# Kernel optimization log

Hardware: AMD Instinct MI355X
Metric: run time of the kernel (lower is better)

## Reference

```python
import jax, jax.numpy as jnp
import numpy as np
import math

D = 2048
H = 16
DH = D // H
DFF = 8192
B = 4
S = 2048
EPS = 1e-12


def gelu(x):
    # faithful tanh-approx gelu from source
    return 0.5 * x * (1.0 + jnp.tanh(math.sqrt(2.0 / math.pi) * (x + 0.044715 * x ** 3)))


def global_layernorm(x, w, b):
    # torch.mean(x)/torch.var(x): scalar mean and UNBIASED variance over ALL elements
    mean = jnp.mean(x)
    var = jnp.var(x, ddof=1)
    return (x - mean) / jnp.sqrt(var + EPS) * w + b


def setup_inputs() -> dict:
    key = jax.random.key(0)
    ks = jax.random.split(key, 12)
    sd = 0.02
    return {
        "x": jax.random.normal(ks[0], (B, S, D), jnp.float32),
        "W1_w": jax.random.normal(ks[1], (3 * D, D), jnp.float32) * sd,
        "W1_b": jnp.zeros((3 * D,), jnp.float32),
        "W2_w": jax.random.normal(ks[2], (D, D), jnp.float32) * sd,
        "W2_b": jnp.zeros((D,), jnp.float32),
        "fc_w": jax.random.normal(ks[3], (DFF, D), jnp.float32) * sd,
        "fc_b": jnp.zeros((DFF,), jnp.float32),
        "proj_w": jax.random.normal(ks[4], (D, DFF), jnp.float32) * sd,
        "proj_b": jnp.zeros((D,), jnp.float32),
        "ln1_w": jnp.ones((D,), jnp.float32),
        "ln1_b": jnp.zeros((D,), jnp.float32),
        "ln2_w": jnp.ones((D,), jnp.float32),
        "ln2_b": jnp.zeros((D,), jnp.float32),
    }


def attn(x, W1_w, W1_b, W2_w, W2_b):
    X = x @ W1_w.T + W1_b                     # [B,S,3D]
    Q, K, V = jnp.split(X, 3, axis=2)         # each [B,S,D]
    # reshape(): view (B,S,H,Dh) then permute
    q = Q.reshape(B, S, H, DH).transpose(0, 2, 3, 1)  # [B,H,Dh,S]
    k = K.reshape(B, S, H, DH).transpose(0, 2, 1, 3)  # [B,H,S,Dh]
    v = V.reshape(B, S, H, DH).transpose(0, 2, 3, 1)  # [B,H,Dh,S]
    # heads(): scores over head-feature dim, scaled by sqrt(q.size(-1)) = sqrt(S)
    w = jnp.einsum('bhds,bhse->bhde', q, k) / math.sqrt(S)  # [B,H,Dh,Dh]
    w = jax.nn.softmax(w, axis=-1)
    out = jnp.einsum('bhde,bhes->bhds', w, v)  # [B,H,Dh,S]
    # cat(): raw contiguous view [B,H,Dh,S] -> [B,S,H*Dh] (memory-order reshape)
    out = out.reshape(B, S, H * DH)
    return out @ W2_w.T + W2_b


def ffn(x, fc_w, fc_b, proj_w, proj_b):
    h = gelu(x @ fc_w.T + fc_b)
    return h @ proj_w.T + proj_b


def reference(x, W1_w, W1_b, W2_w, W2_b, fc_w, fc_b, proj_w, proj_b,
              ln1_w, ln1_b, ln2_w, ln2_b):
    a = attn(x, W1_w, W1_b, W2_w, W2_b)
    x = global_layernorm(a + x, ln1_w, ln1_b)
    m = ffn(x, fc_w, fc_b, proj_w, proj_b)
    x = global_layernorm(m + x, ln2_w, ln2_b)
    return x
```

## Files before the change

kernel.cpp:

```cpp
#include <hip/hip_runtime.h>
#include <math.h>

typedef float floatx4 __attribute__((ext_vector_type(4)));
typedef __bf16 bf16x8 __attribute__((ext_vector_type(8)));
typedef unsigned short ushortx8 __attribute__((ext_vector_type(8)));
typedef unsigned short ushortx4 __attribute__((ext_vector_type(4)));
typedef unsigned short ushortx2 __attribute__((ext_vector_type(2)));

typedef unsigned int __attribute__((address_space(1))) as1_uint;
typedef unsigned int __attribute__((address_space(3))) as3_uint;

#define DEV static __device__ __forceinline__

DEV unsigned short f32_bf16(float f) {
  unsigned u = __float_as_uint(f);
  u += 0x7FFFu + ((u >> 16) & 1u);
  return (unsigned short)(u >> 16);
}
DEV float bf16_f32(unsigned short h) { return __uint_as_float(((unsigned)h) << 16); }
DEV float gelu_f(float x) {
  float x3 = x * x * x;
  return 0.5f * x * (1.0f + tanhf(0.79788456080286536f * (x + 0.044715f * x3)));
}
DEV void gload16(const void* g, void* l) {
  __builtin_amdgcn_global_load_lds((const as1_uint*)g, (as3_uint*)l, 16, 0, 0);
}
DEV floatx4 mfma16(ushortx8 a, ushortx8 b, floatx4 c) {
  return __builtin_amdgcn_mfma_f32_16x16x32_bf16(
      __builtin_bit_cast(bf16x8, a), __builtin_bit_cast(bf16x8, b), c, 0, 0, 0);
}


__global__ void zero_f(float* p, int n) {
  int i = threadIdx.x;
  if (i < n) p[i] = 0.f;
}

__global__ void cvt_f32_bf16(const float* __restrict__ in, unsigned short* __restrict__ out,
                             long n4) {
  long i = (long)blockIdx.x * blockDim.x + threadIdx.x;
  if (i >= n4) return;
  float4 v = ((const float4*)in)[i];
  ushortx4 o;
  o.x = f32_bf16(v.x); o.y = f32_bf16(v.y); o.z = f32_bf16(v.z); o.w = f32_bf16(v.w);
  ((ushortx4*)out)[i] = o;
}

__global__ void cvt_cols(const float* __restrict__ in, unsigned short* __restrict__ out,
                         int cbase, int cwlog4, long n4) {
  long i = (long)blockIdx.x * blockDim.x + threadIdx.x;
  if (i >= n4) return;
  int n = (int)(i >> cwlog4);
  int k4 = (int)(i & ((1 << cwlog4) - 1)) << 2;
  float4 v = *(const float4*)&in[(size_t)n * 8192 + cbase + k4];
  ushortx4 o;
  o.x = f32_bf16(v.x); o.y = f32_bf16(v.y); o.z = f32_bf16(v.z); o.w = f32_bf16(v.w);
  *(ushortx4*)&out[((size_t)n << (cwlog4 + 2)) + k4] = o;
}

__global__ __launch_bounds__(256) void softmax_k(const float* __restrict__ sc,
                                                 unsigned short* __restrict__ probs) {
  int r = blockIdx.x * 4 + (threadIdx.x >> 6);
  int lane = threadIdx.x & 63;
  size_t base = (size_t)(r >> 7) * 16384 + (size_t)(r & 127) * 128;
  int e0 = lane * 2;
  float2 p = *(const float2*)&sc[base + e0];
  const float scale = 0.022097086912079608f;
  float vx = p.x * scale, vy = p.y * scale;
  float m = fmaxf(vx, vy);
#pragma unroll
  for (int off = 32; off; off >>= 1) m = fmaxf(m, __shfl_xor(m, off));
  float ex = expf(vx - m), ey = expf(vy - m);
  float s = ex + ey;
#pragma unroll
  for (int off = 32; off; off >>= 1) s += __shfl_xor(s, off);
  float inv = 1.f / s;
  ushortx2 o;
  o.x = f32_bf16(ex * inv);
  o.y = f32_bf16(ey * inv);
  *(ushortx2*)&probs[base + e0] = o;
}

__global__ void ln_apply(const float* __restrict__ r, const float* __restrict__ stats,
                         const float* __restrict__ w, const float* __restrict__ bia,
                         float* __restrict__ outF, unsigned short* __restrict__ outB, long n4) {
  long i = (long)blockIdx.x * blockDim.x + threadIdx.x;
  if (i >= n4) return;
  const double total = 16777216.0;
  double mean = (double)stats[0] / total;
  double var = ((double)stats[1] - total * mean * mean) / (total - 1.0);
  float rstd = (float)(1.0 / sqrt(var + 1e-12));
  float fm = (float)mean;
  int col = (int)((i * 4) & 2047);
  float4 v = ((const float4*)r)[i];
  float4 wv = *(const float4*)&w[col];
  float4 bv = *(const float4*)&bia[col];
  float4 o;
  o.x = (v.x - fm) * rstd * wv.x + bv.x;
  o.y = (v.y - fm) * rstd * wv.y + bv.y;
  o.z = (v.z - fm) * rstd * wv.z + bv.z;
  o.w = (v.w - fm) * rstd * wv.w + bv.w;
  if (outF) ((float4*)outF)[i] = o;
  if (outB) {
    ushortx4 ob;
    ob.x = f32_bf16(o.x); ob.y = f32_bf16(o.y); ob.z = f32_bf16(o.z); ob.w = f32_bf16(o.w);
    ((ushortx4*)outB)[i] = ob;
  }
}

__global__ __launch_bounds__(256) void gemm_bt(
    const unsigned short* __restrict__ A, int lda, long sAo, long sAi,
    const unsigned short* __restrict__ B, int ldb, long sBo, long sBi,
    int K, int innerCnt,
    const float* __restrict__ bias, const float* __restrict__ residF,
    const unsigned short* __restrict__ residB, int accum,
    float* __restrict__ outF, unsigned short* __restrict__ outB,
    unsigned short* __restrict__ outQT,
    int ldc, long sCo, long sCi, int doGelu, float* __restrict__ stats) {
  __shared__ unsigned short As[128 * 64];
  __shared__ unsigned short Bs[128 * 64];
  const int tid = threadIdx.x;
  const int wave = tid >> 6;
  const int lane = tid & 63;
  const int z = blockIdx.z;
  const int zo = z / innerCnt, zi = z % innerCnt;
  const unsigned short* Ab = A + zo * sAo + zi * sAi;
  const unsigned short* Bb = B + zo * sBo + zi * sBi;
  const long coff = zo * sCo + zi * sCi;
  const int m0 = blockIdx.y * 128;
  const int n0 = blockIdx.x * 128;

  const int quad = lane >> 4;
  const int l16 = lane & 15;
  const int wm = (wave & 1) * 64;
  const int wn = (wave >> 1) * 64;
  const int srow = lane >> 3;
  const int kofs8 = (((lane & 7) ^ srow) & 7) * 8;

  floatx4 acc[4][4];
#pragma unroll
  for (int i = 0; i < 4; i++)
#pragma unroll
    for (int j = 0; j < 4; j++) acc[i][j] = (floatx4){0.f, 0.f, 0.f, 0.f};

  const int nK = K >> 6;
  for (int kt = 0; kt < nK; ++kt) {
    const int k0 = kt << 6;
    __syncthreads();
#pragma unroll
    for (int i = 0; i < 4; ++i) {
      const int rb = wave * 32 + i * 8;
      gload16(Ab + (size_t)(m0 + rb + srow) * lda + k0 + kofs8, &As[rb * 64]);
      gload16(Bb + (size_t)(n0 + rb + srow) * ldb + k0 + kofs8, &Bs[rb * 64]);
    }
    __syncthreads();
#pragma unroll
    for (int kk = 0; kk < 2; ++kk) {
      ushortx8 af[4], bf[4];
      const int swz = (l16 & 7);
#pragma unroll
      for (int i = 0; i < 4; i++)
        af[i] = *(const ushortx8*)&As[(wm + i * 16 + l16) * 64 +
                                      (((kk * 4 + quad) ^ swz) * 8)];
#pragma unroll
      for (int j = 0; j < 4; j++)
        bf[j] = *(const ushortx8*)&Bs[(wn + j * 16 + l16) * 64 +
                                      (((kk * 4 + quad) ^ swz) * 8)];
#pragma unroll
      for (int i = 0; i < 4; i++)
#pragma unroll
        for (int j = 0; j < 4; j++) acc[i][j] = mfma16(af[i], bf[j], acc[i][j]);
    }
  }

  float s1 = 0.f, s2 = 0.f;
#pragma unroll
  for (int i = 0; i < 4; i++) {
#pragma unroll
    for (int j = 0; j < 4; j++) {
      const int col = n0 + wn + j * 16 + l16;
      const float bv = bias ? bias[col] : 0.f;
#pragma unroll
      for (int r = 0; r < 4; r++) {
        const int row = m0 + wm + i * 16 + quad * 4 + r;
        float v = acc[i][j][r] + bv;
        if (doGelu) v = gelu_f(v);
        if (outQT) {
          const int b = row >> 11, s = row & 2047;
          if (col < 4096) {
            unsigned short* tb = outQT + ((col & 2048) ? 16777216u : 0u);
            const int cc = col & 2047;
            tb[((size_t)((b << 4) + (cc >> 7)) * 128 + (cc & 127)) * 2048 + s] = f32_bf16(v);
          } else {
            outB[(size_t)row * 2048 + (col - 4096)] = f32_bf16(v);
          }
          continue;
        }
        const size_t cidx = (size_t)coff + (size_t)row * ldc + col;
        if (residF) v += residF[cidx];
        if (residB) v += bf16_f32(residB[cidx]);
        if (accum) v += outF[cidx];
        if (outF) outF[cidx] = v;
        else outB[cidx] = f32_bf16(v);
        if (stats) { s1 += v; s2 += v * v; }
      }
    }
  }
  if (stats) {
#pragma unroll
    for (int off = 32; off; off >>= 1) {
      s1 += __shfl_down(s1, off);
      s2 += __shfl_down(s2, off);
    }
    if (lane == 0) {
      atomicAdd(&stats[0], s1);
      atomicAdd(&stats[1], s2);
    }
  }
}

__global__ __launch_bounds__(512, 2) void gemm256(
    const unsigned short* __restrict__ A, int lda,
    const unsigned short* __restrict__ B, int ldb, int K,
    const float* __restrict__ bias, const float* __restrict__ residF,
    const unsigned short* __restrict__ residB, int accum,
    float* __restrict__ outF, unsigned short* __restrict__ outB,
    unsigned short* __restrict__ outQT, int ldc, int doGelu,
    float* __restrict__ stats) {
  __shared__ unsigned short As[2][256 * 64];
  __shared__ unsigned short Bs[2][256 * 64];
  const int tid = threadIdx.x;
  const int wave = tid >> 6;
  const int lane = tid & 63;
  const int wm = wave >> 2;
  const int wn = wave & 3;
  const int quad = lane >> 4;
  const int l16 = lane & 15;
  const int swz = l16 & 7;

  const int nwg = gridDim.x * gridDim.y;
  const int orig = blockIdx.y * gridDim.x + blockIdx.x;
  const int q8 = nwg >> 3, r8 = nwg & 7;
  const int xcd = orig & 7, lid = orig >> 3;
  const int wgid = (xcd < r8 ? xcd * (q8 + 1) : r8 * (q8 + 1) + (xcd - r8) * q8) + lid;
  const int m0 = (wgid / gridDim.x) * 256;
  const int n0 = (wgid % gridDim.x) * 256;

  const int srow = lane >> 3;
  const int kof = (((lane & 7) ^ srow) & 7) << 3;
  const int nkt = K >> 6;

  floatx4 acc[8][4];
#pragma unroll
  for (int i = 0; i < 8; i++)
#pragma unroll
    for (int j = 0; j < 4; j++) acc[i][j] = (floatx4){0.f, 0.f, 0.f, 0.f};

  auto slot = [&](int kt, int s) {
    const int buf = kt & 1;
    const int k0 = kt << 6;
    if (s < 2) {
      const int rb = s * 128 + wave * 16;
      gload16(B + (size_t)(n0 + rb + srow) * ldb + k0 + kof, &Bs[buf][rb * 64]);
      gload16(B + (size_t)(n0 + rb + 8 + srow) * ldb + k0 + kof, &Bs[buf][(rb + 8) * 64]);
    } else {
      const int rb = ((wave & 4) << 5) + ((wave & 3) << 4) + (s == 3 ? 64 : 0);
      gload16(A + (size_t)(m0 + rb + srow) * lda + k0 + kof, &As[buf][rb * 64]);
      gload16(A + (size_t)(m0 + rb + 8 + srow) * lda + k0 + kof, &As[buf][(rb + 8) * 64]);
    }
  };

  slot(0, 0); slot(0, 1); slot(0, 2); slot(0, 3);
  if (nkt > 1) { slot(1, 0); slot(1, 1); slot(1, 2); }
  asm volatile("s_waitcnt vmcnt(6)" ::: "memory");
  __builtin_amdgcn_s_barrier();
  asm volatile("" ::: "memory");

  ushortx8 bfr[4][2], afr[2][2];
  const int aBase = (wm * 128 + l16) * 64;
  const int bBase = (wn * 64 + l16) * 64;
  const int kq0 = (quad ^ swz) << 3;
  const int kq1 = ((4 + quad) ^ swz) << 3;

  for (int kt = 0; kt < nkt; kt += 2) {
#pragma unroll
    for (int half = 0; half < 2; half++) {
      const unsigned short* Asb = &As[half][0];
      const unsigned short* Bsb = &Bs[half][0];
#pragma unroll
      for (int p = 0; p < 4; p++) {
        if (p == 0) {
#pragma unroll
          for (int fj = 0; fj < 4; fj++) {
            bfr[fj][0] = *(const ushortx8*)&Bsb[bBase + fj * 1024 + kq0];
            bfr[fj][1] = *(const ushortx8*)&Bsb[bBase + fj * 1024 + kq1];
          }
        }
#pragma unroll
        for (int fi = 0; fi < 2; fi++) {
          afr[fi][0] = *(const ushortx8*)&Asb[aBase + (p * 2 + fi) * 1024 + kq0];
          afr[fi][1] = *(const ushortx8*)&Asb[aBase + (p * 2 + fi) * 1024 + kq1];
        }
        if (half == 0) {
          if (p == 0) { if (kt + 1 < nkt) slot(kt + 1, 3); }
          else { if (kt + 2 < nkt) slot(kt + 2, p - 1); }
        } else {
          if (p == 0) { if (kt + 2 < nkt) slot(kt + 2, 3); }
          else { if (kt + 3 < nkt) slot(kt + 3, p - 1); }
        }
        __builtin_amdgcn_s_barrier();
        asm volatile("s_waitcnt lgkmcnt(0)" ::: "memory");
        __builtin_amdgcn_s_setprio(1);
#pragma unroll
        for (int fi = 0; fi < 2; fi++)
#pragma unroll
          for (int fj = 0; fj < 4; fj++) {
            acc[p * 2 + fi][fj] = mfma16(afr[fi][0], bfr[fj][0], acc[p * 2 + fi][fj]);
            acc[p * 2 + fi][fj] = mfma16(afr[fi][1], bfr[fj][1], acc[p * 2 + fi][fj]);
          }
        __builtin_amdgcn_s_setprio(0);
        if (p == 3) {
          const bool more = (half == 0) ? (kt + 2 < nkt) : (kt + 3 < nkt);
          if (more) asm volatile("s_waitcnt vmcnt(6)" ::: "memory");
          else asm volatile("s_waitcnt vmcnt(0)" ::: "memory");
        }
        __builtin_amdgcn_s_barrier();
        asm volatile("" ::: "memory");
      }
    }
  }

  float s1 = 0.f, s2 = 0.f;
#pragma unroll
  for (int i = 0; i < 8; i++) {
#pragma unroll
    for (int j = 0; j < 4; j++) {
      const int col = n0 + wn * 64 + j * 16 + l16;
      const float bv = bias ? bias[col] : 0.f;
#pragma unroll
      for (int r = 0; r < 4; r++) {
        const int row = m0 + wm * 128 + i * 16 + quad * 4 + r;
        float v = acc[i][j][r] + bv;
        if (doGelu) v = gelu_f(v);
        if (outQT) {
          const int b = row >> 11, s = row & 2047;
          if (col < 4096) {
            unsigned short* tb = outQT + ((col & 2048) ? 16777216u : 0u);
            const int cc = col & 2047;
            tb[((size_t)((b << 4) + (cc >> 7)) * 128 + (cc & 127)) * 2048 + s] = f32_bf16(v);
          } else {
            outB[(size_t)row * 2048 + (col - 4096)] = f32_bf16(v);
          }
          continue;
        }
        const size_t cidx = (size_t)row * ldc + col;
        if (residF) v += residF[cidx];
        if (residB) v += bf16_f32(residB[cidx]);
        if (accum) v += outF[cidx];
        if (outF) outF[cidx] = v;
        else outB[cidx] = f32_bf16(v);
        if (stats) { s1 += v; s2 += v * v; }
      }
    }
  }
  if (stats) {
#pragma unroll
    for (int off = 32; off; off >>= 1) {
      s1 += __shfl_down(s1, off);
      s2 += __shfl_down(s2, off);
    }
    if (lane == 0) {
      atomicAdd(&stats[0], s1);
      atomicAdd(&stats[1], s2);
    }
  }
}


extern "C" void kernel_launch(void* const* d_in, const int* in_sizes, int n_in, void* d_out,
                              int out_size, void* d_ws, size_t ws_size, hipStream_t stream) {
  (void)in_sizes; (void)n_in; (void)out_size;
  const float* x    = (const float*)d_in[0];
  const float* W1w  = (const float*)d_in[1];
  const float* W1b  = (const float*)d_in[2];
  const float* W2w  = (const float*)d_in[3];
  const float* W2b  = (const float*)d_in[4];
  const float* fcw  = (const float*)d_in[5];
  const float* fcb  = (const float*)d_in[6];
  const float* pjw  = (const float*)d_in[7];
  const float* pjb  = (const float*)d_in[8];
  const float* ln1w = (const float*)d_in[9];
  const float* ln1b = (const float*)d_in[10];
  const float* ln2w = (const float*)d_in[11];
  const float* ln2b = (const float*)d_in[12];
  float* out = (float*)d_out;

  char* ws = (char*)d_ws;
  size_t off = 0;
  auto take = [&](size_t b) { size_t r = off; off = (off + b + 255) & ~(size_t)255; return r; };
  float* stats = (float*)(ws + take(256));
  size_t P0 = take(33554432);
  size_t P1 = take(25165824);
  size_t P2 = take(100663296);
  size_t P3 = off;

  unsigned short* xbf    = (unsigned short*)(ws + P0);
  unsigned short* attnbf = (unsigned short*)(ws + P0);
  unsigned short* W1bf   = (unsigned short*)(ws + P1);
  float*          spart  = (float*)(ws + P1);
  unsigned short* probs  = (unsigned short*)(ws + P1 + 4194304);
  unsigned short* W2bf   = (unsigned short*)(ws + P1);
  unsigned short* vbf    = (unsigned short*)(ws + P2);
  unsigned short* qT     = (unsigned short*)(ws + P2 + 33554432);
  float*          r12    = (float*)(ws + P2);
  unsigned short* x1bf   = (unsigned short*)(ws + P2 + 67108864);

  int nc;
  unsigned short *fc_ch, *pj_ch, *hch;
  if (ws_size >= P3 + 201326592) {
    nc = 1;
    fc_ch = (unsigned short*)(ws + P3);
    pj_ch = (unsigned short*)(ws + P3 + 33554432);
    hch   = (unsigned short*)(ws + P3 + 67108864);
  } else if (ws_size >= P3 + 100663296) {
    nc = 2;
    fc_ch = (unsigned short*)(ws + P3);
    pj_ch = (unsigned short*)(ws + P3 + 16777216);
    hch   = (unsigned short*)(ws + P3 + 33554432);
  } else {
    nc = 4;
    fc_ch = (unsigned short*)(ws + P1);
    pj_ch = (unsigned short*)(ws + P1 + 8388608);
    hch   = (unsigned short*)(ws + P0);
  }
  const int cw = 8192 / nc;
  const int cwlog4 = (nc == 1) ? 11 : (nc == 2) ? 10 : 9;
  const long cn4 = (long)cw << 9;

  zero_f<<<1, 64, 0, stream>>>(stats, 16);
  cvt_f32_bf16<<<16384, 256, 0, stream>>>(x, xbf, 4194304);
  cvt_f32_bf16<<<12288, 256, 0, stream>>>(W1w, W1bf, 3145728);

  gemm256<<<dim3(24, 32, 1), 512, 0, stream>>>(xbf, 2048, W1bf, 2048, 2048, W1b, nullptr,
                                               nullptr, 0, nullptr, vbf, qT, 0, 0, nullptr);
  gemm_bt<<<dim3(1, 1, 64), 256, 0, stream>>>(qT, 2048, 0, 262144L, qT + 16777216, 2048, 0,
                                              262144L, 2048, 64, nullptr, nullptr, nullptr, 0,
                                              spart, nullptr, nullptr, 128, 0, 16384L, 0, nullptr);
  softmax_k<<<2048, 256, 0, stream>>>(spart, probs);
  gemm_bt<<<dim3(16, 1, 64), 256, 0, stream>>>(probs, 128, 262144L, 16384L, vbf, 2048, 4194304L,
                                               128L, 128, 16, nullptr, nullptr, nullptr, 0,
                                               nullptr, attnbf, nullptr, 2048, 4194304L, 262144L,
                                               0, nullptr);
  cvt_f32_bf16<<<4096, 256, 0, stream>>>(W2w, W2bf, 1048576);
  gemm256<<<dim3(8, 32, 1), 512, 0, stream>>>(attnbf, 2048, W2bf, 2048, 2048, W2b, x, nullptr,
                                              0, r12, nullptr, nullptr, 2048, 0, stats);
  ln_apply<<<16384, 256, 0, stream>>>(r12, stats, ln1w, ln1b, nullptr, x1bf, 4194304);

  for (int c = 0; c < nc; ++c) {
    cvt_f32_bf16<<<(int)(cn4 / 256), 256, 0, stream>>>(fcw + (size_t)c * cw * 2048, fc_ch, cn4);
    cvt_cols<<<(int)(cn4 / 256), 256, 0, stream>>>(pjw, pj_ch, c * cw, cwlog4, cn4);
    gemm256<<<dim3(cw / 256, 32, 1), 512, 0, stream>>>(x1bf, 2048, fc_ch, 2048, 2048,
                                                       fcb + c * cw, nullptr, nullptr, 0,
                                                       nullptr, hch, nullptr, cw, 1, nullptr);
    const int last = (c == nc - 1);
    gemm256<<<dim3(8, 32, 1), 512, 0, stream>>>(hch, cw, pj_ch, cw, cw,
                                                last ? pjb : nullptr, nullptr,
                                                last ? x1bf : nullptr, c > 0, r12, nullptr,
                                                nullptr, 2048, 0,
                                                last ? (stats + 2) : nullptr);
  }
  ln_apply<<<16384, 256, 0, stream>>>(r12, stats + 2, ln2w, ln2b, out, nullptr, 4194304);
}
```

Measured before the change: 1.596 ms.

## Split-K score GEMM, LDS-transposed QKV epilogue, grouped tile order, finer vmcnt waits

Several independent changes. The Q·K^T score GEMM is split four ways along the sequence dimension (256 workgroups instead of 64), and the softmax kernel sums the four partial results. The QKV GEMM epilogue now transposes Q/K tiles through LDS so the transposed bf16 output is written as coalesced 16-byte stores instead of scattered 2-byte stores. The GEMM also gets a grouped tile-to-workgroup mapping for L2 reuse, finer-grained vmcnt waits with the lgkmcnt wait removed, and a sigmoid-form GELU using a fast exp and reciprocal. The risks are extra partial-score traffic and slightly different GELU rounding.

```diff
diff --git a/kernel.cpp b/kernel.cpp
--- a/kernel.cpp
+++ b/kernel.cpp
@@ -19,8 +19,8 @@
 }
 DEV float bf16_f32(unsigned short h) { return __uint_as_float(((unsigned)h) << 16); }
 DEV float gelu_f(float x) {
-  float x3 = x * x * x;
-  return 0.5f * x * (1.0f + tanhf(0.79788456080286536f * (x + 0.044715f * x3)));
+  float t2 = 1.5957691216057308f * (x + 0.044715f * x * x * x);
+  return x * __builtin_amdgcn_rcpf(1.0f + __expf(-t2));
 }
 DEV void gload16(const void* g, void* l) {
   __builtin_amdgcn_global_load_lds((const as1_uint*)g, (as3_uint*)l, 16, 0, 0);
@@ -62,11 +62,14 @@
                                                  unsigned short* __restrict__ probs) {
   int r = blockIdx.x * 4 + (threadIdx.x >> 6);
   int lane = threadIdx.x & 63;
-  size_t base = (size_t)(r >> 7) * 16384 + (size_t)(r & 127) * 128;
-  int e0 = lane * 2;
-  float2 p = *(const float2*)&sc[base + e0];
+  size_t base = (size_t)(r >> 7) * 16384 + (size_t)(r & 127) * 128 + lane * 2;
+  float2 p0 = *(const float2*)&sc[base];
+  float2 p1 = *(const float2*)&sc[base + 1048576];
+  float2 p2 = *(const float2*)&sc[base + 2097152];
+  float2 p3 = *(const float2*)&sc[base + 3145728];
   const float scale = 0.022097086912079608f;
-  float vx = p.x * scale, vy = p.y * scale;
+  float vx = (p0.x + p1.x + p2.x + p3.x) * scale;
+  float vy = (p0.y + p1.y + p2.y + p3.y) * scale;
   float m = fmaxf(vx, vy);
 #pragma unroll
   for (int off = 32; off; off >>= 1) m = fmaxf(m, __shfl_xor(m, off));
@@ -78,7 +81,7 @@
   ushortx2 o;
   o.x = f32_bf16(ex * inv);
   o.y = f32_bf16(ey * inv);
-  *(ushortx2*)&probs[base + e0] = o;
+  *(ushortx2*)&probs[base] = o;
 }
 
 __global__ void ln_apply(const float* __restrict__ r, const float* __restrict__ stats,
@@ -243,8 +246,15 @@
   const int q8 = nwg >> 3, r8 = nwg & 7;
   const int xcd = orig & 7, lid = orig >> 3;
   const int wgid = (xcd < r8 ? xcd * (q8 + 1) : r8 * (q8 + 1) + (xcd - r8) * q8) + lid;
-  const int m0 = (wgid / gridDim.x) * 256;
-  const int n0 = (wgid % gridDim.x) * 256;
+  int m0, n0;
+  if ((gridDim.x & 7) == 0) {
+    const int gper = (int)(gridDim.y << 3);
+    m0 = ((wgid % gper) >> 3) * 256;
+    n0 = (((wgid / gper) << 3) + (wgid & 7)) * 256;
+  } else {
+    m0 = (wgid / gridDim.x) * 256;
+    n0 = (wgid % gridDim.x) * 256;
+  }
 
   const int srow = lane >> 3;
   const int kof = (((lane & 7) ^ srow) & 7) << 3;
@@ -283,6 +293,8 @@
   const int kq1 = ((4 + quad) ^ swz) << 3;
 
   for (int kt = 0; kt < nkt; kt += 2) {
+    const int m2 = (kt + 2 < nkt);
+    const int m3 = (kt + 3 < nkt);
 #pragma unroll
     for (int half = 0; half < 2; half++) {
       const unsigned short* Asb = &As[half][0];
@@ -303,13 +315,14 @@
         }
         if (half == 0) {
           if (p == 0) { if (kt + 1 < nkt) slot(kt + 1, 3); }
-          else { if (kt + 2 < nkt) slot(kt + 2, p - 1); }
+          else if (m2) slot(kt + 2, p - 1);
         } else {
-          if (p == 0) { if (kt + 2 < nkt) slot(kt + 2, 3); }
-          else { if (kt + 3 < nkt) slot(kt + 3, p - 1); }
-        }
+          if (p == 0) { if (m2) slot(kt + 2, 3); }
+          else if (m3) slot(kt + 3, p - 1);
+        }
+        asm volatile("" ::: "memory");
         __builtin_amdgcn_s_barrier();
-        asm volatile("s_waitcnt lgkmcnt(0)" ::: "memory");
+        asm volatile("" ::: "memory");
         __builtin_amdgcn_s_setprio(1);
 #pragma unroll
         for (int fi = 0; fi < 2; fi++)
@@ -319,15 +332,77 @@
             acc[p * 2 + fi][fj] = mfma16(afr[fi][1], bfr[fj][1], acc[p * 2 + fi][fj]);
           }
         __builtin_amdgcn_s_setprio(0);
-        if (p == 3) {
-          const bool more = (half == 0) ? (kt + 2 < nkt) : (kt + 3 < nkt);
-          if (more) asm volatile("s_waitcnt vmcnt(6)" ::: "memory");
-          else asm volatile("s_waitcnt vmcnt(0)" ::: "memory");
-        }
+        if (p == 1) {
+          if (half == 0) {
+            if (m2) asm volatile("s_waitcnt vmcnt(10)" ::: "memory");
+            else    asm volatile("s_waitcnt vmcnt(8)" ::: "memory");
+          } else {
+            if (m3) asm volatile("s_waitcnt vmcnt(10)" ::: "memory");
+            else    asm volatile("s_waitcnt vmcnt(0)" ::: "memory");
+          }
+        } else if (p == 3) {
+          if (half == 0) {
+            if (m2) asm volatile("s_waitcnt vmcnt(8)" ::: "memory");
+            else    asm volatile("s_waitcnt vmcnt(2)" ::: "memory");
+          } else {
+            if (m3) asm volatile("s_waitcnt vmcnt(8)" ::: "memory");
+            else    asm volatile("s_waitcnt vmcnt(0)" ::: "memory");
+          }
+        }
+        asm volatile("" ::: "memory");
         __builtin_amdgcn_s_barrier();
         asm volatile("" ::: "memory");
       }
     }
+  }
+
+  if (outQT) {
+    if (n0 < 4096) {
+      unsigned short* trb = (wave < 4) ? (unsigned short*)&As[0][0] + wave * 8192
+                                       : (unsigned short*)&Bs[0][0] + (wave - 4) * 8192;
+#pragma unroll
+      for (int j = 0; j < 4; j++) {
+        const int c = j * 16 + l16;
+        const float bv = bias ? bias[n0 + wn * 64 + c] : 0.f;
+#pragma unroll
+        for (int i = 0; i < 8; i++) {
+          ushortx4 o;
+          o.x = f32_bf16(acc[i][j][0] + bv);
+          o.y = f32_bf16(acc[i][j][1] + bv);
+          o.z = f32_bf16(acc[i][j][2] + bv);
+          o.w = f32_bf16(acc[i][j][3] + bv);
+          *(ushortx4*)&trb[c * 128 + (((i * 4 + quad) ^ (c & 6)) << 2)] = o;
+        }
+      }
+      const int bb = m0 >> 11;
+      const int sbase = (m0 & 2047) + wm * 128;
+      unsigned short* tb = outQT + ((n0 & 2048) ? 16777216u : 0u);
+      const int cg = lane >> 4;
+      const int sl = lane & 15;
+#pragma unroll
+      for (int it = 0; it < 16; it++) {
+        const int c = it * 4 + cg;
+        ushortx8 v = *(const ushortx8*)&trb[c * 128 + (((2 * sl) ^ (c & 6)) << 2)];
+        const int cc = (n0 + wn * 64 + c) & 2047;
+        unsigned short* dst = tb +
+            ((size_t)((bb << 4) + (cc >> 7)) * 128 + (cc & 127)) * 2048 + sbase + sl * 8;
+        *(ushortx8*)dst = v;
+      }
+    } else {
+#pragma unroll
+      for (int i = 0; i < 8; i++)
+#pragma unroll
+        for (int j = 0; j < 4; j++) {
+          const int col = n0 + wn * 64 + j * 16 + l16;
+          const float bv = bias ? bias[col] : 0.f;
+#pragma unroll
+          for (int r = 0; r < 4; r++) {
+            const int row = m0 + wm * 128 + i * 16 + quad * 4 + r;
+            outB[(size_t)row * 2048 + (col - 4096)] = f32_bf16(acc[i][j][r] + bv);
+          }
+        }
+    }
+    return;
   }
 
   float s1 = 0.f, s2 = 0.f;
@@ -342,17 +417,6 @@
         const int row = m0 + wm * 128 + i * 16 + quad * 4 + r;
         float v = acc[i][j][r] + bv;
         if (doGelu) v = gelu_f(v);
-        if (outQT) {
-          const int b = row >> 11, s = row & 2047;
-          if (col < 4096) {
-            unsigned short* tb = outQT + ((col & 2048) ? 16777216u : 0u);
-            const int cc = col & 2047;
-            tb[((size_t)((b << 4) + (cc >> 7)) * 128 + (cc & 127)) * 2048 + s] = f32_bf16(v);
-          } else {
-            outB[(size_t)row * 2048 + (col - 4096)] = f32_bf16(v);
-          }
-          continue;
-        }
         const size_t cidx = (size_t)row * ldc + col;
         if (residF) v += residF[cidx];
         if (residB) v += bf16_f32(residB[cidx]);
@@ -408,7 +472,7 @@
   unsigned short* attnbf = (unsigned short*)(ws + P0);
   unsigned short* W1bf   = (unsigned short*)(ws + P1);
   float*          spart  = (float*)(ws + P1);
-  unsigned short* probs  = (unsigned short*)(ws + P1 + 4194304);
+  unsigned short* probs  = (unsigned short*)(ws + P1 + 16777216);
   unsigned short* W2bf   = (unsigned short*)(ws + P1);
   unsigned short* vbf    = (unsigned short*)(ws + P2);
   unsigned short* qT     = (unsigned short*)(ws + P2 + 33554432);
@@ -443,9 +507,10 @@
 
   gemm256<<<dim3(24, 32, 1), 512, 0, stream>>>(xbf, 2048, W1bf, 2048, 2048, W1b, nullptr,
                                                nullptr, 0, nullptr, vbf, qT, 0, 0, nullptr);
-  gemm_bt<<<dim3(1, 1, 64), 256, 0, stream>>>(qT, 2048, 0, 262144L, qT + 16777216, 2048, 0,
-                                              262144L, 2048, 64, nullptr, nullptr, nullptr, 0,
-                                              spart, nullptr, nullptr, 128, 0, 16384L, 0, nullptr);
+  gemm_bt<<<dim3(1, 1, 256), 256, 0, stream>>>(qT, 2048, 262144L, 512L, qT + 16777216, 2048,
+                                               262144L, 512L, 512, 4, nullptr, nullptr, nullptr,
+                                               0, spart, nullptr, nullptr, 128, 16384L, 1048576L,
+                                               0, nullptr);
   softmax_k<<<2048, 256, 0, stream>>>(spart, probs);
   gemm_bt<<<dim3(16, 1, 64), 256, 0, stream>>>(probs, 128, 262144L, 16384L, vbf, 2048, 4194304L,
                                                128L, 128, 16, nullptr, nullptr, nullptr, 0,
```

After: 1.346 ms. 1.19x faster.
